# Performance work log

Hardware: AMD Instinct MI355X
Metric: run time of the kernel (lower is better)

The kernel has to match this reference:

```python
import jax, jax.numpy as jnp
import numpy as np

EMBED_DIM = 1024
NHEAD = 16
HEAD_DIM = EMBED_DIM // NHEAD  # 64
B, S = 2, 2048


def _rotate_half(x):
    x1, x2 = jnp.split(x, 2, axis=-1)
    return jnp.concatenate([-x2, x1], axis=-1)


def _apply_rope(t, cos, sin):
    # t: (B, H, S, Dh); cos/sin: (S, Dh) broadcast over leading dims
    return t * cos + _rotate_half(t) * sin


def setup_inputs() -> dict:
    key = jax.random.key(0)
    ks = jax.random.split(key, 6)
    x = jax.random.normal(ks[0], (B, S, EMBED_DIM), dtype=jnp.float32)
    # real RoPE tables: theta_i = 10000^(-2i/Dh), duplicated for the two halves
    inv_freq = 1.0 / (10000.0 ** (jnp.arange(0, HEAD_DIM, 2, dtype=jnp.float32) / HEAD_DIM))
    freqs = jnp.outer(jnp.arange(S, dtype=jnp.float32), inv_freq)  # (S, Dh/2)
    emb = jnp.concatenate([freqs, freqs], axis=-1)  # (S, Dh)
    cos = jnp.cos(emb)
    sin = jnp.sin(emb)
    W_in = jax.random.normal(ks[1], (EMBED_DIM, 3 * EMBED_DIM), dtype=jnp.float32) * 0.02
    b_in = jax.random.normal(ks[2], (3 * EMBED_DIM,), dtype=jnp.float32) * 0.02
    W_out = jax.random.normal(ks[3], (EMBED_DIM, EMBED_DIM), dtype=jnp.float32) * 0.02
    b_out = jax.random.normal(ks[4], (EMBED_DIM,), dtype=jnp.float32) * 0.02
    return {"x": x, "cos": cos, "sin": sin, "W_in": W_in, "b_in": b_in,
            "W_out": W_out, "b_out": b_out}


def reference(x, cos, sin, W_in, b_in, W_out, b_out):
    Bs, Ss, D = x.shape
    qkv = x @ W_in + b_in  # (B, S, 3D)
    q, k, v = jnp.split(qkv, 3, axis=-1)
    # (B, S, D) -> (B, H, S, Dh)
    def heads(t):
        return t.reshape(Bs, Ss, NHEAD, HEAD_DIM).transpose(0, 2, 1, 3)
    q, k, v = heads(q), heads(k), heads(v)
    q = _apply_rope(q, cos, sin)
    k = _apply_rope(k, cos, sin)
    scale = 1.0 / jnp.sqrt(jnp.array(HEAD_DIM, dtype=x.dtype))
    scores = jnp.einsum('bhqd,bhkd->bhqk', q, k) * scale
    attn = jax.nn.softmax(scores, axis=-1)
    out = jnp.einsum('bhqk,bhkd->bhqd', attn, v)
    out = out.transpose(0, 2, 1, 3).reshape(Bs, Ss, D)
    return out @ W_out + b_out
```

## Files before the change

kernel.cpp:

```cpp
#include <hip/hip_runtime.h>
#include <hip/hip_bf16.h>

typedef float f32x4 __attribute__((ext_vector_type(4)));
typedef short s16x8 __attribute__((ext_vector_type(8)));

typedef const __attribute__((address_space(1))) unsigned int* as1u;
typedef __attribute__((address_space(3))) unsigned int* as3u;

__device__ __forceinline__ unsigned short f2bf(float f) {
    union { float f; unsigned u; } v; v.f = f;
    unsigned u = v.u;
    u += 0x7fffu + ((u >> 16) & 1u);
    return (unsigned short)(u >> 16);
}

__device__ __forceinline__ void gload16(const void* g, void* l3) {
    __builtin_amdgcn_global_load_lds((as1u)g, (as3u)l3, 16, 0, 0);
}

__device__ __forceinline__ int swzo(int row, int cb) {
    return row * 128 + (cb ^ ((row & 7) << 4));
}

#define LOG2E 1.4426950408889634f
#define QSCALE (0.125f * LOG2E)

__global__ __launch_bounds__(256) void prep_kernel(
    const float* __restrict__ x, unsigned short* __restrict__ xb,
    const float* __restrict__ W_in, unsigned short* __restrict__ Wt_in,
    const float* __restrict__ W_out, unsigned short* __restrict__ Wot)
{
    const int t = threadIdx.x;
    int blk = blockIdx.x;
    if (blk < 2048) {
        size_t i = ((size_t)blk * 256 + t) * 8;
        float4 a = *(const float4*)&x[i];
        float4 b = *(const float4*)&x[i + 4];
        s16x8 p;
        p[0] = (short)f2bf(a.x); p[1] = (short)f2bf(a.y);
        p[2] = (short)f2bf(a.z); p[3] = (short)f2bf(a.w);
        p[4] = (short)f2bf(b.x); p[5] = (short)f2bf(b.y);
        p[6] = (short)f2bf(b.z); p[7] = (short)f2bf(b.w);
        *(s16x8*)&xb[i] = p;
        return;
    }
    const float* W;
    unsigned short* Wt;
    int N;
    if (blk < 2816) { blk -= 2048; W = W_in;  Wt = Wt_in; N = 3072; }
    else            { blk -= 2816; W = W_out; Wt = Wot;   N = 1024; }
    __shared__ alignas(16) short T[64 * 64];
    const int KB = 16;
    const int kb = blk % KB, nb = blk / KB;
#pragma unroll
    for (int pass = 0; pass < 4; ++pass) {
        int k = pass * 16 + (t >> 4);
        int n4 = (t & 15) * 4;
        float4 v = *(const float4*)&W[(size_t)(kb * 64 + k) * N + nb * 64 + n4];
        short4 s4;
        s4.x = (short)f2bf(v.x); s4.y = (short)f2bf(v.y);
        s4.z = (short)f2bf(v.z); s4.w = (short)f2bf(v.w);
        *(short4*)((char*)T + k * 128 + ((n4 * 2) ^ ((k & 7) << 4))) = s4;
    }
    __syncthreads();
#pragma unroll
    for (int pass = 0; pass < 4; ++pass) {
        int n = pass * 16 + (t >> 4);
        int k4 = (t & 15) * 4;
        short4 s4;
        s4.x = *(const short*)((const char*)T + (k4 + 0) * 128 + ((n * 2) ^ (((k4 + 0) & 7) << 4)));
        s4.y = *(const short*)((const char*)T + (k4 + 1) * 128 + ((n * 2) ^ (((k4 + 1) & 7) << 4)));
        s4.z = *(const short*)((const char*)T + (k4 + 2) * 128 + ((n * 2) ^ (((k4 + 2) & 7) << 4)));
        s4.w = *(const short*)((const char*)T + (k4 + 3) * 128 + ((n * 2) ^ (((k4 + 3) & 7) << 4)));
        *(short4*)&Wt[(size_t)(nb * 64 + n) * 1024 + kb * 64 + k4] = s4;
    }
}

__global__ __launch_bounds__(512, 2) void qkv_rope_kernel(
    const unsigned short* __restrict__ xb, const unsigned short* __restrict__ Wt,
    const float* __restrict__ bias, const float* __restrict__ cosb,
    const float* __restrict__ sinb,
    unsigned short* __restrict__ Qb, unsigned short* __restrict__ Kb,
    unsigned short* __restrict__ Vb)
{
    __shared__ alignas(16) short As[2][256 * 64];
    __shared__ alignas(16) short Bs[2][256 * 64];
    const int bid = blockIdx.x;
    const int mb = bid & 15, nb = bid >> 4;
    const int t = threadIdx.x, w = t >> 6, l = t & 63;
    const int g = l >> 4, j = l & 15;
    const int wm = w >> 2, wn = w & 3;
    const int m0 = mb * 256, n0 = nb * 256;

    f32x4 acc[8][4];
#pragma unroll
    for (int mi = 0; mi < 8; ++mi)
#pragma unroll
        for (int ni = 0; ni < 4; ++ni) acc[mi][ni] = (f32x4){0.f, 0.f, 0.f, 0.f};

#pragma unroll
    for (int i = 0; i < 4; ++i) {
        int p = (w * 4 + i) * 1024 + l * 16;
        int r = p >> 7, lb = (p & 127) ^ ((r & 7) << 4);
        gload16(&xb[(size_t)(m0 + r) * 1024 + (lb >> 1)], (char*)As[0] + (w * 4 + i) * 1024);
        gload16(&Wt[(size_t)(n0 + r) * 1024 + (lb >> 1)], (char*)Bs[0] + (w * 4 + i) * 1024);
    }
    asm volatile("s_waitcnt vmcnt(0)" ::: "memory");
    __builtin_amdgcn_s_barrier();

    for (int kti = 0; kti < 16; ++kti) {
        const int cur = kti & 1, nxt = cur ^ 1;
        const int ktn = ((kti + 1) & 15) * 64;

#pragma unroll
        for (int i = 0; i < 4; ++i) {
            int p = (w * 4 + i) * 1024 + l * 16;
            int r = p >> 7, lb = (p & 127) ^ ((r & 7) << 4);
            gload16(&xb[(size_t)(m0 + r) * 1024 + ktn + (lb >> 1)], (char*)As[nxt] + (w * 4 + i) * 1024);
            gload16(&Wt[(size_t)(n0 + r) * 1024 + ktn + (lb >> 1)], (char*)Bs[nxt] + (w * 4 + i) * 1024);
        }
        asm volatile("s_waitcnt vmcnt(8)" ::: "memory");
        __builtin_amdgcn_s_barrier();

#pragma unroll
        for (int kf = 0; kf < 2; ++kf) {
            s16x8 bv[4];
#pragma unroll
            for (int ni = 0; ni < 4; ++ni)
                bv[ni] = *(const s16x8*)((const char*)Bs[cur] + swzo(wn * 64 + ni * 16 + j, kf * 64 + g * 16));
#pragma unroll
            for (int mh = 0; mh < 2; ++mh) {
                s16x8 af[4];
#pragma unroll
                for (int mi = 0; mi < 4; ++mi)
                    af[mi] = *(const s16x8*)((const char*)As[cur] + swzo(wm * 128 + mh * 64 + mi * 16 + j, kf * 64 + g * 16));
                __builtin_amdgcn_s_setprio(1);
#pragma unroll
                for (int mi = 0; mi < 4; ++mi)
#pragma unroll
                    for (int ni = 0; ni < 4; ++ni)
                        acc[mh * 4 + mi][ni] = __builtin_amdgcn_mfma_f32_16x16x32_bf16(af[mi], bv[ni], acc[mh * 4 + mi][ni], 0, 0, 0);
                __builtin_amdgcn_s_setprio(0);
            }
        }
        __builtin_amdgcn_s_barrier();
    }

    const int row0 = m0 + wm * 128;
    const int col0 = n0 + wn * 64;
    const int sec = col0 >> 10;
    const int h = (col0 & 1023) >> 6;

    if (sec < 2) {
        unsigned short* dst = (sec == 0) ? Qb : Kb;
        const float qs = (sec == 0) ? QSCALE : 1.0f;
#pragma unroll
        for (int nt = 0; nt < 2; ++nt) {
            const int d = nt * 16 + j;
            const float b1 = bias[col0 + d];
            const float b2 = bias[col0 + d + 32];
#pragma unroll
            for (int mi = 0; mi < 8; ++mi) {
#pragma unroll
                for (int r = 0; r < 4; ++r) {
                    int row = row0 + mi * 16 + g * 4 + r;
                    int s = row & 2047, bb = row >> 11;
                    float c = cosb[s * 64 + d], sn = sinb[s * 64 + d];
                    float x1 = acc[mi][nt][r] + b1;
                    float x2 = acc[mi][nt + 2][r] + b2;
                    float lo = (x1 * c - x2 * sn) * qs;
                    float hi = (x1 * sn + x2 * c) * qs;
                    size_t base = ((size_t)(bb * 16 + h) * 2048 + s) * 64;
                    dst[base + d] = f2bf(lo);
                    dst[base + d + 32] = f2bf(hi);
                }
            }
        }
    } else {
#pragma unroll
        for (int nt = 0; nt < 4; ++nt) {
            const int d = nt * 16 + j;
            const float bvv = bias[col0 + d];
#pragma unroll
            for (int mi = 0; mi < 8; ++mi) {
#pragma unroll
                for (int r = 0; r < 4; ++r) {
                    int row = row0 + mi * 16 + g * 4 + r;
                    int s = row & 2047, bb = row >> 11;
                    size_t base = ((size_t)(bb * 16 + h) * 2048 + s) * 64;
                    Vb[base + d] = f2bf(acc[mi][nt][r] + bvv);
                }
            }
        }
    }
}

#define NROUND 16
__global__ __launch_bounds__(512, 4) void attn_kernel(
    const unsigned short* __restrict__ Qb, const unsigned short* __restrict__ Kb,
    const unsigned short* __restrict__ Vb, unsigned short* __restrict__ AO)
{
    __shared__ alignas(16) short Ks[2][2 * 64 * 64];
    __shared__ alignas(16) short Vt[2][2 * 64 * 64];
    const int bid = blockIdx.x;
    const int bh = (bid & 7) + ((bid >> 7) << 3);
    const int qt = (bid >> 3) & 15;
    const int t = threadIdx.x, w = t >> 6, l = t & 63;
    const int g = l >> 4, j = l & 15;
    const unsigned short* Qh = Qb + (size_t)bh * 131072;
    const unsigned short* Kh = Kb + (size_t)bh * 131072;
    const unsigned short* Vh = Vb + (size_t)bh * 131072;
    const int q0 = qt * 128 + w * 16;

    s16x8 aq[2];
    aq[0] = *(const s16x8*)&Qh[(size_t)(q0 + j) * 64 + g * 8];
    aq[1] = *(const s16x8*)&Qh[(size_t)(q0 + j) * 64 + 32 + g * 8];

    float lt_ = 0.f;
    f32x4 o[4];
#pragma unroll
    for (int dt = 0; dt < 4; ++dt) o[dt] = (f32x4){0.f, 0.f, 0.f, 0.f};

    const bool vrole = (w < 4);
    const int tv = t & 255;
    const int vk = (tv & 31) * 2;
    const int vd = (tv >> 5) * 8;
    const int kw = (w & 3);

    s16x8 va[2], vb2[2];

    if (vrole) {
#pragma unroll
        for (int s = 0; s < 2; ++s) {
            va[s]  = *(const s16x8*)&Vh[(size_t)(s * 64 + vk) * 64 + vd];
            vb2[s] = *(const s16x8*)&Vh[(size_t)(s * 64 + vk + 1) * 64 + vd];
        }
    } else {
#pragma unroll
        for (int i = 0; i < 4; ++i) {
            int p = (kw * 4 + i) * 1024 + l * 16;
            int s = p >> 13, q = p & 8191;
            int r = q >> 7, lb = (q & 127) ^ ((r & 7) << 4);
            gload16(&Kh[(size_t)(s * 64 + r) * 64 + (lb >> 1)],
                    (char*)Ks[0] + (kw * 4 + i) * 1024);
        }
    }
    asm volatile("s_waitcnt vmcnt(0)" ::: "memory");
    if (vrole) {
#pragma unroll
        for (int s = 0; s < 2; ++s)
#pragma unroll
            for (int dd = 0; dd < 8; ++dd) {
                int d = vd + dd;
                unsigned pkv = (unsigned)(unsigned short)va[s][dd] | ((unsigned)(unsigned short)vb2[s][dd] << 16);
                *(unsigned*)((char*)Vt[0] + s * 8192 + d * 128 + ((vk * 2) ^ ((d & 7) << 4))) = pkv;
            }
    }
    asm volatile("s_waitcnt lgkmcnt(0)" ::: "memory");
    __builtin_amdgcn_s_barrier();

    for (int rr = 0; rr < NROUND; ++rr) {
        const int cur = rr & 1, nxt = cur ^ 1;
        const int kvp = ((rr + 1) & (NROUND - 1)) * 128;

        if (vrole) {
#pragma unroll
            for (int s = 0; s < 2; ++s) {
                va[s]  = *(const s16x8*)&Vh[(size_t)(kvp + s * 64 + vk) * 64 + vd];
                vb2[s] = *(const s16x8*)&Vh[(size_t)(kvp + s * 64 + vk + 1) * 64 + vd];
            }
        } else {
#pragma unroll
            for (int i = 0; i < 4; ++i) {
                int p = (kw * 4 + i) * 1024 + l * 16;
                int s = p >> 13, q = p & 8191;
                int r = q >> 7, lb = (q & 127) ^ ((r & 7) << 4);
                gload16(&Kh[(size_t)(kvp + s * 64 + r) * 64 + (lb >> 1)],
                        (char*)Ks[nxt] + (kw * 4 + i) * 1024);
            }
        }

        f32x4 sc[2][4];
#pragma unroll
        for (int sub = 0; sub < 2; ++sub)
#pragma unroll
            for (int nt = 0; nt < 4; ++nt) sc[sub][nt] = (f32x4){0.f, 0.f, 0.f, 0.f};
        __builtin_amdgcn_s_setprio(1);
#pragma unroll
        for (int sub = 0; sub < 2; ++sub) {
            const char* kbase = (const char*)Ks[cur] + sub * 8192;
#pragma unroll
            for (int kf = 0; kf < 2; ++kf) {
                s16x8 bk[4];
#pragma unroll
                for (int nt = 0; nt < 4; ++nt)
                    bk[nt] = *(const s16x8*)(kbase + swzo(nt * 16 + j, kf * 64 + g * 16));
#pragma unroll
                for (int nt = 0; nt < 4; ++nt)
                    sc[sub][nt] = __builtin_amdgcn_mfma_f32_16x16x32_bf16(bk[nt], aq[kf], sc[sub][nt], 0, 0, 0);
            }
        }
        __builtin_amdgcn_s_setprio(0);

#pragma unroll
        for (int sub = 0; sub < 2; ++sub) {
            const char* vbase = (const char*)Vt[cur] + sub * 8192;

            float rs = 0.f;
#pragma unroll
            for (int nt = 0; nt < 4; ++nt)
#pragma unroll
                for (int r = 0; r < 4; ++r) {
                    sc[sub][nt][r] = __builtin_amdgcn_exp2f(sc[sub][nt][r]);
                    rs += sc[sub][nt][r];
                }
            lt_ += rs;

            unsigned pk[4][2];
#pragma unroll
            for (int nt = 0; nt < 4; ++nt)
#pragma unroll
                for (int s = 0; s < 2; ++s)
                    asm("v_cvt_pk_bf16_f32 %0, %1, %2"
                        : "=v"(pk[nt][s]) : "v"(sc[sub][nt][2 * s]), "v"(sc[sub][nt][2 * s + 1]));

#pragma unroll
            for (int kf = 0; kf < 2; ++kf) {
                unsigned A0 = pk[2 * kf][0], A1 = pk[2 * kf][1];
                unsigned B0 = pk[2 * kf + 1][0], B1 = pk[2 * kf + 1][1];
                asm("v_permlane32_swap_b32 %0, %1" : "+v"(A0), "+v"(B0));
                asm("v_permlane32_swap_b32 %0, %1" : "+v"(A1), "+v"(B1));
                asm("v_permlane16_swap_b32 %0, %1" : "+v"(A0), "+v"(B0));
                asm("v_permlane16_swap_b32 %0, %1" : "+v"(A1), "+v"(B1));
                union { unsigned u[4]; s16x8 v; } fr;
                fr.u[0] = A0;
                fr.u[1] = A1;
                fr.u[2] = B0;
                fr.u[3] = B1;
                __builtin_amdgcn_s_setprio(1);
#pragma unroll
                for (int dt = 0; dt < 4; ++dt) {
                    s16x8 vb = *(const s16x8*)(vbase + swzo(dt * 16 + j, kf * 64 + g * 16));
                    o[dt] = __builtin_amdgcn_mfma_f32_16x16x32_bf16(fr.v, vb, o[dt], 0, 0, 0);
                }
                __builtin_amdgcn_s_setprio(0);
            }
        }

        if (vrole) {
#pragma unroll
            for (int s = 0; s < 2; ++s)
#pragma unroll
                for (int dd = 0; dd < 8; ++dd) {
                    int d = vd + dd;
                    unsigned pkv = (unsigned)(unsigned short)va[s][dd] | ((unsigned)(unsigned short)vb2[s][dd] << 16);
                    *(unsigned*)((char*)Vt[nxt] + s * 8192 + d * 128 + ((vk * 2) ^ ((d & 7) << 4))) = pkv;
                }
        }
        asm volatile("s_waitcnt vmcnt(0) lgkmcnt(0)" ::: "memory");
        __builtin_amdgcn_s_barrier();
    }

    lt_ += __shfl_xor(lt_, 16);
    lt_ += __shfl_xor(lt_, 32);

    const int b = bh >> 4, h = bh & 15;
#pragma unroll
    for (int r = 0; r < 4; ++r) {
        float inv = 1.0f / __shfl(lt_, g * 4 + r);
        int s = q0 + g * 4 + r;
        size_t base = ((size_t)b * 2048 + s) * 1024 + h * 64;
#pragma unroll
        for (int dt = 0; dt < 4; ++dt)
            AO[base + dt * 16 + j] = f2bf(o[dt][r] * inv);
    }
}

__global__ __launch_bounds__(256) void out_gemm_kernel(
    const unsigned short* __restrict__ A, const unsigned short* __restrict__ Wot,
    const float* __restrict__ bias, float* __restrict__ out)
{
    __shared__ alignas(16) short As[128 * 64];
    __shared__ alignas(16) short Bs[128 * 64];
    const int bid = blockIdx.x;
    const int xcd = bid & 7, ii = bid >> 3;
    const int mb = (xcd & 3) * 8 + (ii & 7);
    const int nb = (xcd >> 2) * 4 + (ii >> 3);
    const int t = threadIdx.x, w = t >> 6, l = t & 63;
    const int g = l >> 4, j = l & 15;
    const int wm = w >> 1, wn = w & 1;
    const int m0 = mb * 128, n0 = nb * 128;

    f32x4 acc[4][4];
#pragma unroll
    for (int mi = 0; mi < 4; ++mi)
#pragma unroll
        for (int ni = 0; ni < 4; ++ni) acc[mi][ni] = (f32x4){0.f, 0.f, 0.f, 0.f};

    for (int kt = 0; kt < 1024; kt += 64) {
#pragma unroll
        for (int i = 0; i < 4; ++i) {
            int pos = (w * 4 + i) * 1024 + l * 16;
            int r = pos >> 7;
            int lb = (pos & 127) ^ ((r & 7) << 4);
            gload16(&A[(size_t)(m0 + r) * 1024 + kt + (lb >> 1)],
                    (char*)As + (w * 4 + i) * 1024);
            gload16(&Wot[(size_t)(n0 + r) * 1024 + kt + (lb >> 1)],
                    (char*)Bs + (w * 4 + i) * 1024);
        }
        __syncthreads();
#pragma unroll
        for (int kf = 0; kf < 2; ++kf) {
            s16x8 af[4], bv[4];
#pragma unroll
            for (int mi = 0; mi < 4; ++mi)
                af[mi] = *(const s16x8*)((const char*)As + swzo(wm * 64 + mi * 16 + j, kf * 64 + g * 16));
#pragma unroll
            for (int ni = 0; ni < 4; ++ni)
                bv[ni] = *(const s16x8*)((const char*)Bs + swzo(wn * 64 + ni * 16 + j, kf * 64 + g * 16));
#pragma unroll
            for (int mi = 0; mi < 4; ++mi)
#pragma unroll
                for (int ni = 0; ni < 4; ++ni)
                    acc[mi][ni] = __builtin_amdgcn_mfma_f32_16x16x32_bf16(af[mi], bv[ni], acc[mi][ni], 0, 0, 0);
        }
        __syncthreads();
    }

    const int row0 = m0 + wm * 64;
    const int col0 = n0 + wn * 64;
#pragma unroll
    for (int ni = 0; ni < 4; ++ni) {
        const int col = col0 + ni * 16 + j;
        const float bvv = bias[col];
#pragma unroll
        for (int mi = 0; mi < 4; ++mi)
#pragma unroll
            for (int r = 0; r < 4; ++r) {
                int row = row0 + mi * 16 + g * 4 + r;
                out[(size_t)row * 1024 + col] = acc[mi][ni][r] + bvv;
            }
    }
}

extern "C" void kernel_launch(void* const* d_in, const int* in_sizes, int n_in,
                              void* d_out, int out_size, void* d_ws, size_t ws_size,
                              hipStream_t stream) {
    const float* x     = (const float*)d_in[0];
    const float* cosb  = (const float*)d_in[1];
    const float* sinb  = (const float*)d_in[2];
    const float* W_in  = (const float*)d_in[3];
    const float* b_in  = (const float*)d_in[4];
    const float* W_out = (const float*)d_in[5];
    const float* b_out = (const float*)d_in[6];
    float* out = (float*)d_out;

    const size_t HBUF = 2ull * 16 * 2048 * 64;
    if (ws_size < (4 * HBUF + 1024 * 1024) * sizeof(unsigned short)) return;
    unsigned short* Qb = (unsigned short*)d_ws;
    unsigned short* Kb = Qb + HBUF;
    unsigned short* Vb = Kb + HBUF;
    unsigned short* R  = Vb + HBUF;
    unsigned short* Wt_in = R;
    unsigned short* AO    = R;
    unsigned short* Wot   = R + HBUF;
    unsigned short* xbuf  = (unsigned short*)d_out;

    hipLaunchKernelGGL(prep_kernel, dim3(3072), dim3(256), 0, stream,
                       x, xbuf, W_in, Wt_in, W_out, Wot);
    hipLaunchKernelGGL(qkv_rope_kernel, dim3(192), dim3(512), 0, stream,
                       xbuf, Wt_in, b_in, cosb, sinb, Qb, Kb, Vb);
    hipLaunchKernelGGL(attn_kernel, dim3(512), dim3(512), 0, stream,
                       Qb, Kb, Vb, AO);
    hipLaunchKernelGGL(out_gemm_kernel, dim3(256), dim3(256), 0, stream,
                       AO, Wot, b_out, out);
}
```

Measured before the change: 119.8 us.

## Double-buffer LDS tiles in output projection GEMM to overlap loads with MFMA

The output projection GEMM now keeps two LDS buffers for the A and W tiles and prefetches the next K-tile while computing on the current one. It waits on vmcnt(8) instead of draining all loads, and raises wave priority around the MFMA block. This is meant to hide global-to-LDS load latency behind matrix math, at the cost of twice the LDS per block. The last iteration wraps around and fetches a redundant tile, and the launch bounds now request 2 blocks per CU.

Measured after the change: 119.0 us, median of 2. No clear change (-0.7%).

```diff
diff --git a/kernel.cpp b/kernel.cpp
--- a/kernel.cpp
+++ b/kernel.cpp
@@ -376,12 +376,12 @@
     }
 }
 
-__global__ __launch_bounds__(256) void out_gemm_kernel(
+__global__ __launch_bounds__(256, 2) void out_gemm_kernel(
     const unsigned short* __restrict__ A, const unsigned short* __restrict__ Wot,
     const float* __restrict__ bias, float* __restrict__ out)
 {
-    __shared__ alignas(16) short As[128 * 64];
-    __shared__ alignas(16) short Bs[128 * 64];
+    __shared__ alignas(16) short As[2][128 * 64];
+    __shared__ alignas(16) short Bs[2][128 * 64];
     const int bid = blockIdx.x;
     const int xcd = bid & 7, ii = bid >> 3;
     const int mb = (xcd & 3) * 8 + (ii & 7);
@@ -397,34 +397,48 @@
 #pragma unroll
         for (int ni = 0; ni < 4; ++ni) acc[mi][ni] = (f32x4){0.f, 0.f, 0.f, 0.f};
 
-    for (int kt = 0; kt < 1024; kt += 64) {
+#pragma unroll
+    for (int i = 0; i < 4; ++i) {
+        int p = (w * 4 + i) * 1024 + l * 16;
+        int r = p >> 7, lb = (p & 127) ^ ((r & 7) << 4);
+        gload16(&A[(size_t)(m0 + r) * 1024 + (lb >> 1)], (char*)As[0] + (w * 4 + i) * 1024);
+        gload16(&Wot[(size_t)(n0 + r) * 1024 + (lb >> 1)], (char*)Bs[0] + (w * 4 + i) * 1024);
+    }
+    asm volatile("s_waitcnt vmcnt(0)" ::: "memory");
+    __builtin_amdgcn_s_barrier();
+
+    for (int kti = 0; kti < 16; ++kti) {
+        const int cur = kti & 1, nxt = cur ^ 1;
+        const int ktn = ((kti + 1) & 15) * 64;
+
 #pragma unroll
         for (int i = 0; i < 4; ++i) {
-            int pos = (w * 4 + i) * 1024 + l * 16;
-            int r = pos >> 7;
-            int lb = (pos & 127) ^ ((r & 7) << 4);
-            gload16(&A[(size_t)(m0 + r) * 1024 + kt + (lb >> 1)],
-                    (char*)As + (w * 4 + i) * 1024);
-            gload16(&Wot[(size_t)(n0 + r) * 1024 + kt + (lb >> 1)],
-                    (char*)Bs + (w * 4 + i) * 1024);
-        }
-        __syncthreads();
+            int p = (w * 4 + i) * 1024 + l * 16;
+            int r = p >> 7, lb = (p & 127) ^ ((r & 7) << 4);
+            gload16(&A[(size_t)(m0 + r) * 1024 + ktn + (lb >> 1)], (char*)As[nxt] + (w * 4 + i) * 1024);
+            gload16(&Wot[(size_t)(n0 + r) * 1024 + ktn + (lb >> 1)], (char*)Bs[nxt] + (w * 4 + i) * 1024);
+        }
+        asm volatile("s_waitcnt vmcnt(8)" ::: "memory");
+        __builtin_amdgcn_s_barrier();
+
 #pragma unroll
         for (int kf = 0; kf < 2; ++kf) {
             s16x8 af[4], bv[4];
 #pragma unroll
             for (int mi = 0; mi < 4; ++mi)
-                af[mi] = *(const s16x8*)((const char*)As + swzo(wm * 64 + mi * 16 + j, kf * 64 + g * 16));
+                af[mi] = *(const s16x8*)((const char*)As[cur] + swzo(wm * 64 + mi * 16 + j, kf * 64 + g * 16));
 #pragma unroll
             for (int ni = 0; ni < 4; ++ni)
-                bv[ni] = *(const s16x8*)((const char*)Bs + swzo(wn * 64 + ni * 16 + j, kf * 64 + g * 16));
+                bv[ni] = *(const s16x8*)((const char*)Bs[cur] + swzo(wn * 64 + ni * 16 + j, kf * 64 + g * 16));
+            __builtin_amdgcn_s_setprio(1);
 #pragma unroll
             for (int mi = 0; mi < 4; ++mi)
 #pragma unroll
                 for (int ni = 0; ni < 4; ++ni)
                     acc[mi][ni] = __builtin_amdgcn_mfma_f32_16x16x32_bf16(af[mi], bv[ni], acc[mi][ni], 0, 0, 0);
-        }
-        __syncthreads();
+            __builtin_amdgcn_s_setprio(0);
+        }
+        __builtin_amdgcn_s_barrier();
     }
 
     const int row0 = m0 + wm * 64;
```
